# Kernel tuning notes

Hardware: AMD Instinct MI355X
Metric: run time of the kernel (lower is better)

The kernel has to match this reference:

```python
import jax, jax.numpy as jnp
import numpy as np

N = 100000      # number of nodes
FT = 256        # ft_in (hidden units)
NB_CLASSES = 16 # nb_classes
EPS = 1e-8      # torch.cosine_similarity eps


def setup_inputs() -> dict:
    key = jax.random.key(0)
    ks = jax.random.split(key, 7)
    seq = jax.random.normal(ks[0], (N, FT), dtype=jnp.float32)
    seq1 = jax.random.normal(ks[1], (N, FT), dtype=jnp.float32)
    labels = jax.random.randint(ks[2], (N,), 0, NB_CLASSES, dtype=jnp.int32)
    prompt1 = jax.random.normal(ks[3], (1, FT), dtype=jnp.float32)
    prompt2 = jax.random.normal(ks[4], (1, FT), dtype=jnp.float32)
    prompt3 = jax.random.normal(ks[5], (1, FT), dtype=jnp.float32)
    # weighted_prompt.reset_parameters: fixed init 0.5, 0.4, 0.3
    w_wp = jnp.array([[0.5, 0.4, 0.3]], dtype=jnp.float32)
    # weighted_feature.reset_parameters: fixed init 0.0, 1.0
    w_wf = jnp.array([[0.0, 1.0]], dtype=jnp.float32)
    # downstreamprompt.weight: xavier_uniform on [1, ft_in]
    bound = float(np.sqrt(6.0 / (1 + FT)))
    w_dp = jax.random.uniform(ks[6], (1, FT), jnp.float32, -bound, bound)
    a4 = jnp.array([0.1], dtype=jnp.float32)
    return {"seq": seq, "seq1": seq1, "labels": labels,
            "prompt1": prompt1, "prompt2": prompt2, "prompt3": prompt3,
            "w_wp": w_wp, "w_wf": w_wf, "w_dp": w_dp, "a4": a4}


def reference(seq, seq1, labels, prompt1, prompt2, prompt3, w_wp, w_wf, w_dp, a4):
    # weight = 1 + ELU(weighted_prompt(prompt))  -> [1, FT]
    prompt = jnp.concatenate([prompt1, prompt2, prompt3], axis=0)  # [3, FT]
    weight = 1.0 + jax.nn.elu(w_wp @ prompt)                       # [1, FT]
    rawret1 = weight * seq                                          # [N, FT]
    rawret2 = w_dp * seq                                            # downstreamprompt
    rawret3 = jax.nn.elu(w_wf[0, 0] * rawret1 + w_wf[0, 1] * rawret2)
    rawret = rawret3 + a4[0] * seq1                                 # [N, FT]
    # averageemb (train=1 path): per-class mean, zero-count classes stay 0
    sums = jax.ops.segment_sum(rawret, labels, num_segments=NB_CLASSES)  # [C, FT]
    counts = jax.ops.segment_sum(jnp.ones((rawret.shape[0],), rawret.dtype),
                                 labels, num_segments=NB_CLASSES)        # [C]
    ave = jnp.where(counts[:, None] > 0, sums / jnp.maximum(counts, 1.0)[:, None], sums)
    # fused per-pair cosine similarity: normalize + matmul (replaces N*C loop)
    num = rawret @ ave.T                                             # [N, C]
    denom = (jnp.linalg.norm(rawret, axis=1)[:, None] *
             jnp.linalg.norm(ave, axis=1)[None, :])
    ret = num / jnp.maximum(denom, EPS)
    return jax.nn.softmax(ret, axis=1)
```

## Files before the change

kernel.cpp:

```cpp
#include <hip/hip_runtime.h>
#include <hip/hip_bf16.h>

#define NROWS 100000
#define FT 256
#define NC 16
#define NBLK 512

#define FPSCALE 1048576.0f
#define FPINV   (1.0f / 1048576.0f)

#define CW_COEF 0
#define CW_AVEB 256
#define CW_NRM  2304
#define CW_PCNT 2320
#define CW_PART (2320 + NBLK*16)
#define CW_RAWB (CW_PART + NBLK*4096)
#define CW_TOTAL (CW_RAWB + (NROWS*FT)/2)
#define CACHED_NEED_BYTES ((size_t)CW_TOTAL * 4)

#define WS_COEF 0
#define WS_SUMS 256
#define WS_CNTS 4352
#define WS_AVEB 4368
#define WS_NRM  6416

typedef float f32x4 __attribute__((ext_vector_type(4)));
typedef short bf16x8 __attribute__((ext_vector_type(8)));

static __device__ __forceinline__ float bfbits2f(unsigned int u16) {
    union { unsigned int i; float f; } v; v.i = u16 << 16; return v.f;
}
static __device__ __forceinline__ unsigned short f2bf(float f) {
    union { float f; unsigned int i; } v; v.f = f;
    unsigned int u = v.i;
    u += 0x7fffu + ((u >> 16) & 1u);
    return (unsigned short)(u >> 16);
}

__global__ void k_prep(const float* __restrict__ p1,
                       const float* __restrict__ p2,
                       const float* __restrict__ p3,
                       const float* __restrict__ wwp,
                       const float* __restrict__ wwf,
                       const float* __restrict__ wdp,
                       float* __restrict__ ws)
{
    int f = threadIdx.x;
    float z = wwp[0] * p1[f] + wwp[1] * p2[f] + wwp[2] * p3[f];
    float weight = (z > 0.f) ? (1.f + z) : __expf(z);
    ws[CW_COEF + f] = wwf[0] * weight + wwf[1] * wdp[f];
}


__global__ __launch_bounds__(1024) void k_accum_c(
    const float* __restrict__ seq,
    const float* __restrict__ seq1,
    const int* __restrict__ labels,
    const float* __restrict__ a4p,
    float* __restrict__ ws)
{
    __shared__ int lsum[NC * FT];
    __shared__ int lcnt[NC];
    const int tid = threadIdx.x;
    for (int i = tid; i < NC * FT; i += 1024) lsum[i] = 0;
    if (tid < NC) lcnt[tid] = 0;
    __syncthreads();

    const int rr = tid >> 5;
    const int m  = tid & 31;
    const int f0 = m * 8;
    const int mh = m >> 2;
    int off[8];
#pragma unroll
    for (int i = 0; i < 8; ++i) off[i] = (i + mh) & 7;

    float cof[8];
    {
        const float4 c0 = *(const float4*)(ws + CW_COEF + f0);
        const float4 c1 = *(const float4*)(ws + CW_COEF + f0 + 4);
        cof[0]=c0.x; cof[1]=c0.y; cof[2]=c0.z; cof[3]=c0.w;
        cof[4]=c1.x; cof[5]=c1.y; cof[6]=c1.z; cof[7]=c1.w;
    }
    const float a4v = a4p[0];
    unsigned int* rawb = (unsigned int*)(ws + CW_RAWB);

    for (int row = blockIdx.x * 32 + rr; row < NROWS; row += gridDim.x * 32) {
        const int lab = labels[row];
        const float4 sa  = *(const float4*)(seq  + row * FT + f0);
        const float4 sb  = *(const float4*)(seq  + row * FT + f0 + 4);
        const float4 ta  = *(const float4*)(seq1 + row * FT + f0);
        const float4 tb  = *(const float4*)(seq1 + row * FT + f0 + 4);
        const float s[8]  = {sa.x,sa.y,sa.z,sa.w, sb.x,sb.y,sb.z,sb.w};
        const float t[8]  = {ta.x,ta.y,ta.z,ta.w, tb.x,tb.y,tb.z,tb.w};
        int* base = lsum + lab * FT + f0;
        unsigned short vb[8];
#pragma unroll
        for (int i = 0; i < 8; ++i) {
            float u = cof[i] * s[i];
            float r = (u > 0.f) ? u : (__expf(u) - 1.f);
            float v = r + a4v * t[i];
            vb[i] = f2bf(v);
            atomicAdd(base + off[i], __float2int_rn(v * FPSCALE));
        }
        uint4 pk;
        pk.x = (unsigned int)vb[0] | ((unsigned int)vb[1] << 16);
        pk.y = (unsigned int)vb[2] | ((unsigned int)vb[3] << 16);
        pk.z = (unsigned int)vb[4] | ((unsigned int)vb[5] << 16);
        pk.w = (unsigned int)vb[6] | ((unsigned int)vb[7] << 16);
        *(uint4*)(rawb + (row * FT + f0) / 2) = pk;
        if (m == 0) atomicAdd(&lcnt[lab], 1);
    }
    __syncthreads();

    int* gpart = (int*)(ws + CW_PART) + blockIdx.x * (NC * FT);
    for (int idx = tid; idx < NC * FT; idx += 1024) {
        int p  = idx & 255;
        int mm = p >> 3;
        int r  = p & 7;
        int f  = (p & ~7) | ((r - (mm >> 2)) & 7);
        gpart[(idx & ~255) + f] = lsum[idx];
    }
    if (tid < NC) ((int*)(ws + CW_PCNT))[blockIdx.x * NC + tid] = lcnt[tid];
}

__global__ __launch_bounds__(256) void k_reduce(float* __restrict__ ws)
{
    __shared__ float red[256];
    const int c = blockIdx.x;
    const int f = threadIdx.x;

    const int* pcnt = (const int*)(ws + CW_PCNT);
    int cacc = 0;
    for (int p = f; p < NBLK; p += 256) cacc += pcnt[p * NC + c];
    red[f] = (float)cacc;
    __syncthreads();
#pragma unroll
    for (int s = 128; s > 0; s >>= 1) {
        if (f < s) red[f] += red[f + s];
        __syncthreads();
    }
    const float cnt = red[0];
    __syncthreads();

    const int* gpart = (const int*)(ws + CW_PART);
    long long isum = 0;
    for (int p = 0; p < NBLK; ++p)
        isum += (long long)gpart[p * (NC * FT) + c * FT + f];
    float a = ((float)isum * FPINV) / fmaxf(cnt, 1.f);
    unsigned short ab = f2bf(a);
    ((unsigned short*)(ws + CW_AVEB))[c * FT + f] = ab;
    float af = bfbits2f(ab);

    red[f] = af * af;
    __syncthreads();
#pragma unroll
    for (int s = 128; s > 0; s >>= 1) {
        if (f < s) red[f] += red[f + s];
        __syncthreads();
    }
    if (f == 0) ws[CW_NRM + c] = sqrtf(red[0]);
}

__global__ __launch_bounds__(256) void k_out_c(
    const float* __restrict__ ws,
    float* __restrict__ out)
{
    const int tid = threadIdx.x;
    const int lane = tid & 63;
    const int wv   = tid >> 6;
    const int c = lane & 15;
    const int g = lane >> 4;

    const unsigned short* aveb = (const unsigned short*)(ws + CW_AVEB);
    const unsigned short* rawb = (const unsigned short*)(ws + CW_RAWB);
    bf16x8 bfrag[8];
#pragma unroll
    for (int kc = 0; kc < 8; ++kc)
        bfrag[kc] = *(const bf16x8*)(aveb + c * FT + kc * 32 + g * 8);
    const float na = ws[CW_NRM + c];

    const int ntiles = NROWS / 16;
    for (int tile = blockIdx.x * 4 + wv; tile < ntiles; tile += gridDim.x * 4) {
        const int rowbase = tile * 16;
        const int arow = rowbase + c;
        f32x4 accC = {0.f, 0.f, 0.f, 0.f};
        f32x4 accS = {0.f, 0.f, 0.f, 0.f};
#pragma unroll
        for (int kc = 0; kc < 8; ++kc) {
            bf16x8 afrag = *(const bf16x8*)(rawb + arow * FT + kc * 32 + g * 8);
            accC = __builtin_amdgcn_mfma_f32_16x16x32_bf16(afrag, bfrag[kc], accC, 0, 0, 0);
            accS = __builtin_amdgcn_mfma_f32_16x16x32_bf16(afrag, afrag,     accS, 0, 0, 0);
        }
#pragma unroll
        for (int q = 0; q < 4; ++q) {
            const float sd = __shfl(accS[q], g * 20 + q, 64);
            const float nr = sqrtf(fmaxf(sd, 0.f));
            const float denom = fmaxf(nr * na, 1e-8f);
            float cosv = accC[q] / denom;
            float mx = cosv;
#pragma unroll
            for (int o = 1; o < 16; o <<= 1) mx = fmaxf(mx, __shfl_xor(mx, o, 16));
            const float e = __expf(cosv - mx);
            float s = e;
#pragma unroll
            for (int o = 1; o < 16; o <<= 1) s += __shfl_xor(s, o, 16);
            out[(rowbase + g * 4 + q) * NC + c] = e / s;
        }
    }
}


__global__ __launch_bounds__(1024) void k_accum(
    const float* __restrict__ seq,
    const float* __restrict__ seq1,
    const int* __restrict__ labels,
    const float* __restrict__ a4p,
    float* __restrict__ ws)
{
    __shared__ int lsum[NC * FT];
    __shared__ int lcnt[NC];
    const int tid = threadIdx.x;
    for (int i = tid; i < NC * FT; i += 1024) lsum[i] = 0;
    if (tid < NC) lcnt[tid] = 0;
    __syncthreads();

    const int rr = tid >> 5;
    const int m  = tid & 31;
    const int f0 = m * 8;
    const int mh = m >> 2;
    int off[8];
#pragma unroll
    for (int i = 0; i < 8; ++i) off[i] = (i + mh) & 7;

    float cof[8];
    {
        const float4 c0 = *(const float4*)(ws + WS_COEF + f0);
        const float4 c1 = *(const float4*)(ws + WS_COEF + f0 + 4);
        cof[0]=c0.x; cof[1]=c0.y; cof[2]=c0.z; cof[3]=c0.w;
        cof[4]=c1.x; cof[5]=c1.y; cof[6]=c1.z; cof[7]=c1.w;
    }
    const float a4v = a4p[0];

    for (int row = blockIdx.x * 32 + rr; row < NROWS; row += gridDim.x * 32) {
        const int lab = labels[row];
        const float4 sa  = *(const float4*)(seq  + row * FT + f0);
        const float4 sb  = *(const float4*)(seq  + row * FT + f0 + 4);
        const float4 ta  = *(const float4*)(seq1 + row * FT + f0);
        const float4 tb  = *(const float4*)(seq1 + row * FT + f0 + 4);
        const float s[8]  = {sa.x,sa.y,sa.z,sa.w, sb.x,sb.y,sb.z,sb.w};
        const float t[8]  = {ta.x,ta.y,ta.z,ta.w, tb.x,tb.y,tb.z,tb.w};
        int* base = lsum + lab * FT + f0;
#pragma unroll
        for (int i = 0; i < 8; ++i) {
            float u = cof[i] * s[i];
            float r = (u > 0.f) ? u : (__expf(u) - 1.f);
            atomicAdd(base + off[i], __float2int_rn((r + a4v * t[i]) * FPSCALE));
        }
        if (m == 0) atomicAdd(&lcnt[lab], 1);
    }
    __syncthreads();

    int* gsum = (int*)(ws + WS_SUMS);
    for (int idx = tid; idx < NC * FT; idx += 1024) {
        int p  = idx & 255;
        int mm = p >> 3;
        int r  = p & 7;
        int f  = (p & ~7) | ((r - (mm >> 2)) & 7);
        atomicAdd(gsum + (idx & ~255) + f, lsum[idx]);
    }
    if (tid < NC) atomicAdd((int*)(ws + WS_CNTS) + tid, lcnt[tid]);
}

__global__ void k_final(float* __restrict__ ws)
{
    __shared__ float nacc[NC];
    const int f = threadIdx.x;
    if (f < NC) nacc[f] = 0.f;
    __syncthreads();
    const int* gsum = (const int*)(ws + WS_SUMS);
    const int* gcnt = (const int*)(ws + WS_CNTS);
    unsigned short* aveb = (unsigned short*)(ws + WS_AVEB);
#pragma unroll
    for (int c = 0; c < NC; ++c) {
        float cnt = (float)gcnt[c];
        float a = ((float)gsum[c * FT + f] * FPINV) / fmaxf(cnt, 1.f);
        unsigned short ab = f2bf(a);
        aveb[c * FT + f] = ab;
        float af = bfbits2f(ab);
        atomicAdd(&nacc[c], af * af);
    }
    __syncthreads();
    if (f < NC) ws[WS_NRM + f] = sqrtf(nacc[f]);
}

__global__ __launch_bounds__(256) void k_out(
    const float* __restrict__ seq,
    const float* __restrict__ seq1,
    const float* __restrict__ a4p,
    const float* __restrict__ ws,
    float* __restrict__ out)
{
    __shared__ __align__(16) float scoef[FT];
    const int tid = threadIdx.x;
    for (int i = tid; i < FT; i += 256) scoef[i] = ws[WS_COEF + i];
    __syncthreads();

    const int lane = tid & 63;
    const int wv   = tid >> 6;
    const int c = lane & 15;
    const int g = lane >> 4;

    const unsigned short* aveb = (const unsigned short*)(ws + WS_AVEB);
    bf16x8 bfrag[8];
#pragma unroll
    for (int kc = 0; kc < 8; ++kc)
        bfrag[kc] = *(const bf16x8*)(aveb + c * FT + kc * 32 + g * 8);
    const float na  = ws[WS_NRM + c];
    const float a4v = a4p[0];

    const int ntiles = NROWS / 16;
    for (int tile = blockIdx.x * 4 + wv; tile < ntiles; tile += gridDim.x * 4) {
        const int rowbase = tile * 16;
        const int arow = rowbase + c;
        f32x4 accC = {0.f, 0.f, 0.f, 0.f};
        f32x4 accS = {0.f, 0.f, 0.f, 0.f};
#pragma unroll
        for (int kc = 0; kc < 8; ++kc) {
            const int k0 = kc * 32 + g * 8;
            const float4 sa = *(const float4*)(seq  + arow * FT + k0);
            const float4 sb = *(const float4*)(seq  + arow * FT + k0 + 4);
            const float4 ta = *(const float4*)(seq1 + arow * FT + k0);
            const float4 tb = *(const float4*)(seq1 + arow * FT + k0 + 4);
            const float4 c0 = *(const float4*)(scoef + k0);
            const float4 c1 = *(const float4*)(scoef + k0 + 4);
            const float s[8]  = {sa.x,sa.y,sa.z,sa.w, sb.x,sb.y,sb.z,sb.w};
            const float t[8]  = {ta.x,ta.y,ta.z,ta.w, tb.x,tb.y,tb.z,tb.w};
            const float cf[8] = {c0.x,c0.y,c0.z,c0.w, c1.x,c1.y,c1.z,c1.w};
            bf16x8 afrag;
#pragma unroll
            for (int i = 0; i < 8; ++i) {
                float u = cf[i] * s[i];
                float r = (u > 0.f) ? u : (__expf(u) - 1.f);
                afrag[i] = (short)f2bf(r + a4v * t[i]);
            }
            accC = __builtin_amdgcn_mfma_f32_16x16x32_bf16(afrag, bfrag[kc], accC, 0, 0, 0);
            accS = __builtin_amdgcn_mfma_f32_16x16x32_bf16(afrag, afrag,     accS, 0, 0, 0);
        }
#pragma unroll
        for (int q = 0; q < 4; ++q) {
            const float sd = __shfl(accS[q], g * 20 + q, 64);
            const float nr = sqrtf(fmaxf(sd, 0.f));
            const float denom = fmaxf(nr * na, 1e-8f);
            float cosv = accC[q] / denom;
            float mx = cosv;
#pragma unroll
            for (int o = 1; o < 16; o <<= 1) mx = fmaxf(mx, __shfl_xor(mx, o, 16));
            const float e = __expf(cosv - mx);
            float s = e;
#pragma unroll
            for (int o = 1; o < 16; o <<= 1) s += __shfl_xor(s, o, 16);
            out[(rowbase + g * 4 + q) * NC + c] = e / s;
        }
    }
}

extern "C" void kernel_launch(void* const* d_in, const int* in_sizes, int n_in,
                              void* d_out, int out_size, void* d_ws, size_t ws_size,
                              hipStream_t stream)
{
    const float* seq  = (const float*)d_in[0];
    const float* seq1 = (const float*)d_in[1];
    const int*   lab  = (const int*)d_in[2];
    const float* p1   = (const float*)d_in[3];
    const float* p2   = (const float*)d_in[4];
    const float* p3   = (const float*)d_in[5];
    const float* wwp  = (const float*)d_in[6];
    const float* wwf  = (const float*)d_in[7];
    const float* wdp  = (const float*)d_in[8];
    const float* a4   = (const float*)d_in[9];
    float* ws  = (float*)d_ws;
    float* out = (float*)d_out;

    if (ws_size >= CACHED_NEED_BYTES) {
        k_prep   <<<1,    256, 0, stream>>>(p1, p2, p3, wwp, wwf, wdp, ws);
        k_accum_c<<<NBLK, 1024, 0, stream>>>(seq, seq1, lab, a4, ws);
        k_reduce <<<NC,   256, 0, stream>>>(ws);
        k_out_c  <<<1568, 256, 0, stream>>>(ws, out);
    } else {
        hipMemsetAsync((char*)d_ws + WS_SUMS * sizeof(int), 0,
                       (NC * FT + NC) * sizeof(int), stream);
        k_prep <<<1,    256, 0, stream>>>(p1, p2, p3, wwp, wwf, wdp, ws);
        k_accum<<<512, 1024, 0, stream>>>(seq, seq1, lab, a4, ws);
        k_final<<<1,    256, 0, stream>>>(ws);
        k_out  <<<1568, 256, 0, stream>>>(seq, seq1, a4, ws, out);
    }
}
```

Baseline: 292.3 us.

## Fuse prep into accumulate kernel, split partial reduction into two stages

Computes the per-feature coefficients inside each accumulate block's shared memory, which removes the separate prep launch. The accumulate kernel now runs 512-thread blocks that handle two rows per iteration, giving more loads in flight per thread. The single 16-block reduction over 512 partials is replaced by a 128-block first stage over slices and a small second stage, so the reduction is spread across more of the GPU. In exchange there is one extra launch, a redundant coefficient computation in every block, and higher register pressure from the two-row loop.

```diff
diff --git a/kernel.cpp b/kernel.cpp
--- a/kernel.cpp
+++ b/kernel.cpp
@@ -5,16 +5,19 @@
 #define FT 256
 #define NC 16
 #define NBLK 512
+#define NSL 8
+#define SLICE (NBLK / NSL)
 
 #define FPSCALE 1048576.0f
 #define FPINV   (1.0f / 1048576.0f)
 
-#define CW_COEF 0
-#define CW_AVEB 256
-#define CW_NRM  2304
-#define CW_PCNT 2320
-#define CW_PART (2320 + NBLK*16)
-#define CW_RAWB (CW_PART + NBLK*4096)
+#define CW_AVEB 0
+#define CW_NRM  2048
+#define CW_PCNT 2064
+#define CW_ST2C (CW_PCNT + NBLK*NC)
+#define CW_ST2  (CW_ST2C + NSL*NC)
+#define CW_PART (CW_ST2 + NSL*NC*FT)
+#define CW_RAWB (CW_PART + NBLK*NC*FT)
 #define CW_TOTAL (CW_RAWB + (NROWS*FT)/2)
 #define CACHED_NEED_BYTES ((size_t)CW_TOTAL * 4)
 
@@ -36,6 +39,225 @@
     u += 0x7fffu + ((u >> 16) & 1u);
     return (unsigned short)(u >> 16);
 }
+
+
+__global__ __launch_bounds__(512) void k_accum_c(
+    const float* __restrict__ seq,
+    const float* __restrict__ seq1,
+    const int* __restrict__ labels,
+    const float* __restrict__ p1,
+    const float* __restrict__ p2,
+    const float* __restrict__ p3,
+    const float* __restrict__ wwp,
+    const float* __restrict__ wwf,
+    const float* __restrict__ wdp,
+    const float* __restrict__ a4p,
+    float* __restrict__ ws)
+{
+    __shared__ int lsum[NC * FT];
+    __shared__ int lcnt[NC];
+    __shared__ __align__(16) float scoef[FT];
+    const int tid = threadIdx.x;
+    for (int i = tid; i < NC * FT; i += 512) lsum[i] = 0;
+    if (tid < NC) lcnt[tid] = 0;
+    if (tid < FT) {
+        float z = wwp[0] * p1[tid] + wwp[1] * p2[tid] + wwp[2] * p3[tid];
+        float w = (z > 0.f) ? (1.f + z) : __expf(z);
+        scoef[tid] = wwf[0] * w + wwf[1] * wdp[tid];
+    }
+    __syncthreads();
+
+    const int rr = tid >> 5;
+    const int m  = tid & 31;
+    const int f0 = m * 8;
+    const int mh = m >> 2;
+    int off[8];
+#pragma unroll
+    for (int i = 0; i < 8; ++i) off[i] = (i + mh) & 7;
+
+    float cof[8];
+    {
+        const float4 c0 = *(const float4*)(scoef + f0);
+        const float4 c1 = *(const float4*)(scoef + f0 + 4);
+        cof[0]=c0.x; cof[1]=c0.y; cof[2]=c0.z; cof[3]=c0.w;
+        cof[4]=c1.x; cof[5]=c1.y; cof[6]=c1.z; cof[7]=c1.w;
+    }
+    const float a4v = a4p[0];
+    unsigned int* rawb = (unsigned int*)(ws + CW_RAWB);
+
+    const int stride = NBLK * 16;
+    for (int rowA = blockIdx.x * 16 + rr; rowA < NROWS; rowA += stride * 2) {
+        const int rowBr = rowA + stride;
+        const bool vB = rowBr < NROWS;
+        const int rowB = vB ? rowBr : rowA;
+        const int labA = labels[rowA];
+        const int labB = labels[rowB];
+        const float4 saA = *(const float4*)(seq  + rowA * FT + f0);
+        const float4 sbA = *(const float4*)(seq  + rowA * FT + f0 + 4);
+        const float4 taA = *(const float4*)(seq1 + rowA * FT + f0);
+        const float4 tbA = *(const float4*)(seq1 + rowA * FT + f0 + 4);
+        const float4 saB = *(const float4*)(seq  + rowB * FT + f0);
+        const float4 sbB = *(const float4*)(seq  + rowB * FT + f0 + 4);
+        const float4 taB = *(const float4*)(seq1 + rowB * FT + f0);
+        const float4 tbB = *(const float4*)(seq1 + rowB * FT + f0 + 4);
+
+        const float sA[8] = {saA.x,saA.y,saA.z,saA.w, sbA.x,sbA.y,sbA.z,sbA.w};
+        const float tA[8] = {taA.x,taA.y,taA.z,taA.w, tbA.x,tbA.y,tbA.z,tbA.w};
+        const float sB[8] = {saB.x,saB.y,saB.z,saB.w, sbB.x,sbB.y,sbB.z,sbB.w};
+        const float tB[8] = {taB.x,taB.y,taB.z,taB.w, tbB.x,tbB.y,tbB.z,tbB.w};
+
+        int* baseA = lsum + labA * FT + f0;
+        unsigned short vbA[8];
+#pragma unroll
+        for (int i = 0; i < 8; ++i) {
+            float u = cof[i] * sA[i];
+            float r = (u > 0.f) ? u : (__expf(u) - 1.f);
+            float v = r + a4v * tA[i];
+            vbA[i] = f2bf(v);
+            atomicAdd(baseA + off[i], __float2int_rn(v * FPSCALE));
+        }
+        uint4 pkA;
+        pkA.x = (unsigned int)vbA[0] | ((unsigned int)vbA[1] << 16);
+        pkA.y = (unsigned int)vbA[2] | ((unsigned int)vbA[3] << 16);
+        pkA.z = (unsigned int)vbA[4] | ((unsigned int)vbA[5] << 16);
+        pkA.w = (unsigned int)vbA[6] | ((unsigned int)vbA[7] << 16);
+        *(uint4*)(rawb + (rowA * FT + f0) / 2) = pkA;
+        if (m == 0) atomicAdd(&lcnt[labA], 1);
+
+        int* baseB = lsum + labB * FT + f0;
+        unsigned short vbB[8];
+        float vv[8];
+#pragma unroll
+        for (int i = 0; i < 8; ++i) {
+            float u = cof[i] * sB[i];
+            float r = (u > 0.f) ? u : (__expf(u) - 1.f);
+            vv[i] = r + a4v * tB[i];
+            vbB[i] = f2bf(vv[i]);
+        }
+        if (vB) {
+#pragma unroll
+            for (int i = 0; i < 8; ++i)
+                atomicAdd(baseB + off[i], __float2int_rn(vv[i] * FPSCALE));
+            uint4 pkB;
+            pkB.x = (unsigned int)vbB[0] | ((unsigned int)vbB[1] << 16);
+            pkB.y = (unsigned int)vbB[2] | ((unsigned int)vbB[3] << 16);
+            pkB.z = (unsigned int)vbB[4] | ((unsigned int)vbB[5] << 16);
+            pkB.w = (unsigned int)vbB[6] | ((unsigned int)vbB[7] << 16);
+            *(uint4*)(rawb + (rowB * FT + f0) / 2) = pkB;
+            if (m == 0) atomicAdd(&lcnt[labB], 1);
+        }
+    }
+    __syncthreads();
+
+    int* gpart = (int*)(ws + CW_PART) + blockIdx.x * (NC * FT);
+    for (int idx = tid; idx < NC * FT; idx += 512) {
+        int p  = idx & 255;
+        int mm = p >> 3;
+        int r  = p & 7;
+        int f  = (p & ~7) | ((r - (mm >> 2)) & 7);
+        gpart[(idx & ~255) + f] = lsum[idx];
+    }
+    if (tid < NC) ((int*)(ws + CW_PCNT))[blockIdx.x * NC + tid] = lcnt[tid];
+}
+
+__global__ __launch_bounds__(256) void k_reduce1(float* __restrict__ ws)
+{
+    const int c = blockIdx.x >> 3;
+    const int r = blockIdx.x & 7;
+    const int f = threadIdx.x;
+    const int p0 = r * SLICE;
+    const int* gpart = (const int*)(ws + CW_PART);
+    int acc = 0;
+#pragma unroll 8
+    for (int p = 0; p < SLICE; ++p)
+        acc += gpart[(p0 + p) * (NC * FT) + c * FT + f];
+    ((int*)(ws + CW_ST2))[(r * NC + c) * FT + f] = acc;
+
+    if (f < SLICE) {
+        int cc = ((const int*)(ws + CW_PCNT))[(p0 + f) * NC + c];
+#pragma unroll
+        for (int o = 32; o > 0; o >>= 1) cc += __shfl_down(cc, o, 64);
+        if (f == 0) ((int*)(ws + CW_ST2C))[r * NC + c] = cc;
+    }
+}
+
+__global__ __launch_bounds__(256) void k_reduce2(float* __restrict__ ws)
+{
+    __shared__ float red[256];
+    const int c = blockIdx.x;
+    const int f = threadIdx.x;
+    const int* st2  = (const int*)(ws + CW_ST2);
+    const int* st2c = (const int*)(ws + CW_ST2C);
+    long long isum = 0;
+    int cnt = 0;
+#pragma unroll
+    for (int s = 0; s < NSL; ++s) {
+        isum += (long long)st2[(s * NC + c) * FT + f];
+        cnt  += st2c[s * NC + c];
+    }
+    float a = ((float)isum * FPINV) / fmaxf((float)cnt, 1.f);
+    unsigned short ab = f2bf(a);
+    ((unsigned short*)(ws + CW_AVEB))[c * FT + f] = ab;
+    float af = bfbits2f(ab);
+
+    red[f] = af * af;
+    __syncthreads();
+#pragma unroll
+    for (int s = 128; s > 0; s >>= 1) {
+        if (f < s) red[f] += red[f + s];
+        __syncthreads();
+    }
+    if (f == 0) ws[CW_NRM + c] = sqrtf(red[0]);
+}
+
+__global__ __launch_bounds__(256) void k_out_c(
+    const float* __restrict__ ws,
+    float* __restrict__ out)
+{
+    const int tid = threadIdx.x;
+    const int lane = tid & 63;
+    const int wv   = tid >> 6;
+    const int c = lane & 15;
+    const int g = lane >> 4;
+
+    const unsigned short* aveb = (const unsigned short*)(ws + CW_AVEB);
+    const unsigned short* rawb = (const unsigned short*)(ws + CW_RAWB);
+    bf16x8 bfrag[8];
+#pragma unroll
+    for (int kc = 0; kc < 8; ++kc)
+        bfrag[kc] = *(const bf16x8*)(aveb + c * FT + kc * 32 + g * 8);
+    const float na = ws[CW_NRM + c];
+
+    const int ntiles = NROWS / 16;
+    for (int tile = blockIdx.x * 4 + wv; tile < ntiles; tile += gridDim.x * 4) {
+        const int rowbase = tile * 16;
+        const int arow = rowbase + c;
+        f32x4 accC = {0.f, 0.f, 0.f, 0.f};
+        f32x4 accS = {0.f, 0.f, 0.f, 0.f};
+#pragma unroll
+        for (int kc = 0; kc < 8; ++kc) {
+            bf16x8 afrag = *(const bf16x8*)(rawb + arow * FT + kc * 32 + g * 8);
+            accC = __builtin_amdgcn_mfma_f32_16x16x32_bf16(afrag, bfrag[kc], accC, 0, 0, 0);
+            accS = __builtin_amdgcn_mfma_f32_16x16x32_bf16(afrag, afrag,     accS, 0, 0, 0);
+        }
+#pragma unroll
+        for (int q = 0; q < 4; ++q) {
+            const float sd = __shfl(accS[q], g * 20 + q, 64);
+            const float nr = sqrtf(fmaxf(sd, 0.f));
+            const float denom = fmaxf(nr * na, 1e-8f);
+            float cosv = accC[q] / denom;
+            float mx = cosv;
+#pragma unroll
+            for (int o = 1; o < 16; o <<= 1) mx = fmaxf(mx, __shfl_xor(mx, o, 16));
+            const float e = __expf(cosv - mx);
+            float s = e;
+#pragma unroll
+            for (int o = 1; o < 16; o <<= 1) s += __shfl_xor(s, o, 16);
+            out[(rowbase + g * 4 + q) * NC + c] = e / s;
+        }
+    }
+}
+
 
 __global__ void k_prep(const float* __restrict__ p1,
                        const float* __restrict__ p2,
@@ -48,167 +270,8 @@
     int f = threadIdx.x;
     float z = wwp[0] * p1[f] + wwp[1] * p2[f] + wwp[2] * p3[f];
     float weight = (z > 0.f) ? (1.f + z) : __expf(z);
-    ws[CW_COEF + f] = wwf[0] * weight + wwf[1] * wdp[f];
-}
-
-
-__global__ __launch_bounds__(1024) void k_accum_c(
-    const float* __restrict__ seq,
-    const float* __restrict__ seq1,
-    const int* __restrict__ labels,
-    const float* __restrict__ a4p,
-    float* __restrict__ ws)
-{
-    __shared__ int lsum[NC * FT];
-    __shared__ int lcnt[NC];
-    const int tid = threadIdx.x;
-    for (int i = tid; i < NC * FT; i += 1024) lsum[i] = 0;
-    if (tid < NC) lcnt[tid] = 0;
-    __syncthreads();
-
-    const int rr = tid >> 5;
-    const int m  = tid & 31;
-    const int f0 = m * 8;
-    const int mh = m >> 2;
-    int off[8];
-#pragma unroll
-    for (int i = 0; i < 8; ++i) off[i] = (i + mh) & 7;
-
-    float cof[8];
-    {
-        const float4 c0 = *(const float4*)(ws + CW_COEF + f0);
-        const float4 c1 = *(const float4*)(ws + CW_COEF + f0 + 4);
-        cof[0]=c0.x; cof[1]=c0.y; cof[2]=c0.z; cof[3]=c0.w;
-        cof[4]=c1.x; cof[5]=c1.y; cof[6]=c1.z; cof[7]=c1.w;
-    }
-    const float a4v = a4p[0];
-    unsigned int* rawb = (unsigned int*)(ws + CW_RAWB);
-
-    for (int row = blockIdx.x * 32 + rr; row < NROWS; row += gridDim.x * 32) {
-        const int lab = labels[row];
-        const float4 sa  = *(const float4*)(seq  + row * FT + f0);
-        const float4 sb  = *(const float4*)(seq  + row * FT + f0 + 4);
-        const float4 ta  = *(const float4*)(seq1 + row * FT + f0);
-        const float4 tb  = *(const float4*)(seq1 + row * FT + f0 + 4);
-        const float s[8]  = {sa.x,sa.y,sa.z,sa.w, sb.x,sb.y,sb.z,sb.w};
-        const float t[8]  = {ta.x,ta.y,ta.z,ta.w, tb.x,tb.y,tb.z,tb.w};
-        int* base = lsum + lab * FT + f0;
-        unsigned short vb[8];
-#pragma unroll
-        for (int i = 0; i < 8; ++i) {
-            float u = cof[i] * s[i];
-            float r = (u > 0.f) ? u : (__expf(u) - 1.f);
-            float v = r + a4v * t[i];
-            vb[i] = f2bf(v);
-            atomicAdd(base + off[i], __float2int_rn(v * FPSCALE));
-        }
-        uint4 pk;
-        pk.x = (unsigned int)vb[0] | ((unsigned int)vb[1] << 16);
-        pk.y = (unsigned int)vb[2] | ((unsigned int)vb[3] << 16);
-        pk.z = (unsigned int)vb[4] | ((unsigned int)vb[5] << 16);
-        pk.w = (unsigned int)vb[6] | ((unsigned int)vb[7] << 16);
-        *(uint4*)(rawb + (row * FT + f0) / 2) = pk;
-        if (m == 0) atomicAdd(&lcnt[lab], 1);
-    }
-    __syncthreads();
-
-    int* gpart = (int*)(ws + CW_PART) + blockIdx.x * (NC * FT);
-    for (int idx = tid; idx < NC * FT; idx += 1024) {
-        int p  = idx & 255;
-        int mm = p >> 3;
-        int r  = p & 7;
-        int f  = (p & ~7) | ((r - (mm >> 2)) & 7);
-        gpart[(idx & ~255) + f] = lsum[idx];
-    }
-    if (tid < NC) ((int*)(ws + CW_PCNT))[blockIdx.x * NC + tid] = lcnt[tid];
-}
-
-__global__ __launch_bounds__(256) void k_reduce(float* __restrict__ ws)
-{
-    __shared__ float red[256];
-    const int c = blockIdx.x;
-    const int f = threadIdx.x;
-
-    const int* pcnt = (const int*)(ws + CW_PCNT);
-    int cacc = 0;
-    for (int p = f; p < NBLK; p += 256) cacc += pcnt[p * NC + c];
-    red[f] = (float)cacc;
-    __syncthreads();
-#pragma unroll
-    for (int s = 128; s > 0; s >>= 1) {
-        if (f < s) red[f] += red[f + s];
-        __syncthreads();
-    }
-    const float cnt = red[0];
-    __syncthreads();
-
-    const int* gpart = (const int*)(ws + CW_PART);
-    long long isum = 0;
-    for (int p = 0; p < NBLK; ++p)
-        isum += (long long)gpart[p * (NC * FT) + c * FT + f];
-    float a = ((float)isum * FPINV) / fmaxf(cnt, 1.f);
-    unsigned short ab = f2bf(a);
-    ((unsigned short*)(ws + CW_AVEB))[c * FT + f] = ab;
-    float af = bfbits2f(ab);
-
-    red[f] = af * af;
-    __syncthreads();
-#pragma unroll
-    for (int s = 128; s > 0; s >>= 1) {
-        if (f < s) red[f] += red[f + s];
-        __syncthreads();
-    }
-    if (f == 0) ws[CW_NRM + c] = sqrtf(red[0]);
-}
-
-__global__ __launch_bounds__(256) void k_out_c(
-    const float* __restrict__ ws,
-    float* __restrict__ out)
-{
-    const int tid = threadIdx.x;
-    const int lane = tid & 63;
-    const int wv   = tid >> 6;
-    const int c = lane & 15;
-    const int g = lane >> 4;
-
-    const unsigned short* aveb = (const unsigned short*)(ws + CW_AVEB);
-    const unsigned short* rawb = (const unsigned short*)(ws + CW_RAWB);
-    bf16x8 bfrag[8];
-#pragma unroll
-    for (int kc = 0; kc < 8; ++kc)
-        bfrag[kc] = *(const bf16x8*)(aveb + c * FT + kc * 32 + g * 8);
-    const float na = ws[CW_NRM + c];
-
-    const int ntiles = NROWS / 16;
-    for (int tile = blockIdx.x * 4 + wv; tile < ntiles; tile += gridDim.x * 4) {
-        const int rowbase = tile * 16;
-        const int arow = rowbase + c;
-        f32x4 accC = {0.f, 0.f, 0.f, 0.f};
-        f32x4 accS = {0.f, 0.f, 0.f, 0.f};
-#pragma unroll
-        for (int kc = 0; kc < 8; ++kc) {
-            bf16x8 afrag = *(const bf16x8*)(rawb + arow * FT + kc * 32 + g * 8);
-            accC = __builtin_amdgcn_mfma_f32_16x16x32_bf16(afrag, bfrag[kc], accC, 0, 0, 0);
-            accS = __builtin_amdgcn_mfma_f32_16x16x32_bf16(afrag, afrag,     accS, 0, 0, 0);
-        }
-#pragma unroll
-        for (int q = 0; q < 4; ++q) {
-            const float sd = __shfl(accS[q], g * 20 + q, 64);
-            const float nr = sqrtf(fmaxf(sd, 0.f));
-            const float denom = fmaxf(nr * na, 1e-8f);
-            float cosv = accC[q] / denom;
-            float mx = cosv;
-#pragma unroll
-            for (int o = 1; o < 16; o <<= 1) mx = fmaxf(mx, __shfl_xor(mx, o, 16));
-            const float e = __expf(cosv - mx);
-            float s = e;
-#pragma unroll
-            for (int o = 1; o < 16; o <<= 1) s += __shfl_xor(s, o, 16);
-            out[(rowbase + g * 4 + q) * NC + c] = e / s;
-        }
-    }
-}
-
+    ws[WS_COEF + f] = wwf[0] * weight + wwf[1] * wdp[f];
+}
 
 __global__ __launch_bounds__(1024) void k_accum(
     const float* __restrict__ seq,
@@ -382,10 +445,11 @@
     float* out = (float*)d_out;
 
     if (ws_size >= CACHED_NEED_BYTES) {
-        k_prep   <<<1,    256, 0, stream>>>(p1, p2, p3, wwp, wwf, wdp, ws);
-        k_accum_c<<<NBLK, 1024, 0, stream>>>(seq, seq1, lab, a4, ws);
-        k_reduce <<<NC,   256, 0, stream>>>(ws);
-        k_out_c  <<<1568, 256, 0, stream>>>(ws, out);
+        k_accum_c<<<NBLK,     512, 0, stream>>>(seq, seq1, lab, p1, p2, p3,
+                                                wwp, wwf, wdp, a4, ws);
+        k_reduce1<<<NC * NSL, 256, 0, stream>>>(ws);
+        k_reduce2<<<NC,       256, 0, stream>>>(ws);
+        k_out_c  <<<1568,     256, 0, stream>>>(ws, out);
     } else {
         hipMemsetAsync((char*)d_ws + WS_SUMS * sizeof(int), 0,
                        (NC * FT + NC) * sizeof(int), stream);
```

Measured after the change: 270.4 us. 1.08x faster.
